# Optimization experiments

Hardware: AMD Instinct MI355X
Metric: run time of the kernel (lower is better)

## Reference

```python
import jax, jax.numpy as jnp
import numpy as np

CUTOFF = 3.0   # self.cutoff
RMIN = 3.5     # rmin in cutoff_function (note rmin > cutoff, faithful to source)
ETA = 4.0
N_RADIAL = 5
N_3BODY = 12
NATOMS = 2048
K = 48         # neighbors per atom (equal counts -> ragged loop becomes dense batch)
HID = 64
NPAIRS = NATOMS * K


def setup_inputs() -> dict:
    key = jax.random.key(0)
    ks = jax.random.split(key, 4)
    # displacements scaled so |rij| is mostly within a few Angstrom
    rij = jax.random.normal(ks[0], (NPAIRS, 3), jnp.float32) * 1.5
    # sorted-by-atom pair list with K neighbors per atom
    unique_i = jnp.repeat(jnp.arange(NATOMS, dtype=jnp.int64), K)
    W1 = jax.random.normal(ks[1], (N_RADIAL + N_3BODY, HID), jnp.float32) * 0.1
    b1 = jnp.zeros((HID,), jnp.float32)
    W2 = jax.random.normal(ks[2], (HID, HID), jnp.float32) * 0.1
    b2 = jnp.zeros((HID,), jnp.float32)
    W3 = jax.random.normal(ks[3], (HID, 1), jnp.float32) * 0.1
    b3 = jnp.zeros((1,), jnp.float32)
    return dict(rij=rij, unique_i=unique_i, W1=W1, b1=b1, W2=W2, b2=b2, W3=W3, b3=b3)


def _energy(rij, W1, b1, W2, b2, W3, b3):
    d = jnp.linalg.norm(rij, axis=1, keepdims=True)           # (P,1)
    diff_norm = rij / jnp.maximum(d, 1e-12)                   # F.normalize
    # pair cutoff (rmin=3.5, c=3.0 as in source)
    fc = jnp.where(d > RMIN,
                   0.5 + 0.5 * jnp.cos(jnp.pi * (d - RMIN) / (CUTOFF - RMIN)),
                   1.0)
    # radial Bessel basis, n = 1..5
    ns = jnp.arange(1, N_RADIAL + 1, dtype=rij.dtype)
    rbf = jnp.sqrt(2.0 / CUTOFF) * jnp.sin(ns * jnp.pi / CUTOFF * d) / d * fc  # (P,5)
    # 3-body Gaussian descriptors
    fcrik = (0.5 + 0.5 * jnp.cos(jnp.pi * d / CUTOFF))[:, 0]  # (P,)
    dn = diff_norm.reshape(NATOMS, K, 3)
    cosang = jnp.einsum('nkd,nld->nkl', dn, dn)               # (N,K,K) pairwise mm
    cosang = jnp.where(jnp.eye(K, dtype=bool)[None], 0.0, cosang)  # fill_diagonal_(0)
    mu = jnp.linspace(-1.0, 1.0, N_3BODY).astype(rij.dtype)
    w = fcrik.reshape(NATOMS, 1, K, 1)                        # fcrik broadcast on axis being summed
    g3b = jnp.sum(jnp.exp(-ETA * (cosang[..., None] - mu) ** 2) * w, axis=2)  # (N,K,12)
    g3b = g3b.reshape(NPAIRS, N_3BODY)
    desc = jnp.concatenate([rbf, g3b], axis=1)                # (P,17)
    h = jnp.tanh(desc @ W1 + b1)
    h = jnp.tanh(h @ W2 + b2)
    eij = h @ W3 + b3                                         # (P,1)
    return jnp.sum(eij * fc)


def reference(rij, unique_i, W1, b1, W2, b2, W3, b3):
    # Module output: gradients of total energy w.r.t. rij (written into beta)
    return jax.grad(_energy)(rij, W1, b1, W2, b2, W3, b3)
```

## Files before the change

### kernel.cpp

```cpp
#include <hip/hip_runtime.h>
#include <hip/hip_bf16.h>

#define NATOMS 2048
#define K 48
#define P (NATOMS * K)
#define NR 5
#define NM 12
#define ND 17
#define HID 64

#define PI_F 3.14159265358979f
#define CUT 3.0f
#define RMIN_F 3.5f
#define AFC (-6.28318530717959f)
#define POC (PI_F / CUT)
#define SQ 0.816496580927726f
#define E1C 1.45454545454545f
#define CMC (-0.132231404958678f)
#define N4L (-5.77078016355585f)
#define E1L (2.09846551402031f)
#define TL2 (2.88539008177793f)

__device__ unsigned short g_w1t[64 * 32];
__device__ unsigned short g_w2t[64 * 64];
__device__ unsigned short g_w2r[64 * 64];
__device__ unsigned short g_w1r[32 * 64];

using frag_ab = __attribute__((ext_vector_type(8))) short;
using frag_cd = __attribute__((ext_vector_type(4))) float;
using f2 = __attribute__((ext_vector_type(2))) float;
using f4 = __attribute__((ext_vector_type(4))) float;

__device__ __forceinline__ float fast_tanh(float x) {
    const float t = __builtin_amdgcn_exp2f(TL2 * x);
    return 1.0f - 2.0f * __builtin_amdgcn_rcpf(t + 1.0f);
}

__device__ __forceinline__ unsigned short f2bs(float x) {
    __hip_bfloat16 b = __float2bfloat16(x);
    return __builtin_bit_cast(unsigned short, b);
}

__device__ __forceinline__ float bs2f(unsigned short u) {
    return __builtin_bit_cast(float, ((unsigned)u) << 16);
}

template <int CTRL>
__device__ __forceinline__ float dpp_add(float x) {
    const int y = __builtin_amdgcn_update_dpp(
        0, __builtin_bit_cast(int, x), CTRL, 0xF, 0xF, true);
    return x + __builtin_bit_cast(float, y);
}

__global__ __launch_bounds__(256) void k_prep(const float* __restrict__ W1,
                                              const float* __restrict__ W2) {
    const int i = blockIdx.x * 256 + threadIdx.x;
    if (i < 2048) {
        const int n = i >> 5, k = i & 31;
        g_w1t[i] = (k < ND) ? f2bs(W1[k * HID + n]) : (unsigned short)0;
    } else if (i < 2048 + 4096) {
        const int j = i - 2048, n = j >> 6, k = j & 63;
        g_w2t[j] = f2bs(W2[k * HID + n]);
    } else if (i < 2048 + 8192) {
        const int j = i - (2048 + 4096);
        g_w2r[j] = f2bs(W2[j]);
    } else if (i < 2048 + 8192 + 2048) {
        const int j = i - (2048 + 8192), n = j >> 6;
        g_w1r[j] = (n < ND) ? f2bs(W1[j]) : (unsigned short)0;
    }
}

#define H1_OFF   0
#define ST_OFF   0
#define DESC_OFF 6912
#define GZ2_OFF  6912
#define SGD_OFF  6912
#define SGF_OFF  10560
#define SGU_OFF  11328
#define SS_OFF   13824
#define SE_OFF   18528
#define SU_OFF   19296
#define SFC_OFF  20064
#define SFK_OFF  20256
#define SM_BYTES 20448

__global__ __launch_bounds__(256, 6) void k_fused(const float* __restrict__ rij,
                                                  const float* __restrict__ b1,
                                                  const float* __restrict__ b2,
                                                  const float* __restrict__ W3,
                                                  const float* __restrict__ b3,
                                                  float* __restrict__ out) {
    __shared__ __align__(16) char smem[SM_BYTES];
    short*          h1S   = (short*)(smem + H1_OFF);
    unsigned short* sT    = (unsigned short*)(smem + ST_OFF);
    short*          descS = (short*)(smem + DESC_OFF);
    short*          gz2S  = (short*)(smem + GZ2_OFF);
    float*          sgd   = (float*)(smem + SGD_OFF);
    float*          sgf4  = (float*)(smem + SGF_OFF);
    float*          sgu4  = (float*)(smem + SGU_OFF);
    unsigned short* sS    = (unsigned short*)(smem + SS_OFF);
    float*          se    = (float*)(smem + SE_OFF);
    float*          su    = (float*)(smem + SU_OFF);
    float*          sfc   = (float*)(smem + SFC_OFF);
    float*          sfk   = (float*)(smem + SFK_OFF);

    const int t = threadIdx.x;
    const int base3 = blockIdx.x * (K * 3);
    const int w = t >> 6, lane = t & 63, quad = lane >> 4, lm = lane & 15;
    const int n0 = w * 16 + lm;

    const frag_ab wf1  = *(const frag_ab*)&g_w1t[n0 * 32 + quad * 8];
    const frag_ab wf2a = *(const frag_ab*)&g_w2t[n0 * 64 + quad * 8];
    const frag_ab wf2b = *(const frag_ab*)&g_w2t[n0 * 64 + 32 + quad * 8];
    const frag_ab wr2a = *(const frag_ab*)&g_w2r[n0 * 64 + quad * 8];
    const frag_ab wr2b = *(const frag_ab*)&g_w2r[n0 * 64 + 32 + quad * 8];
    const float bias1 = b1[n0];
    const float bias2 = b2[n0];
    const float w3n   = W3[n0];
    const float b3v   = b3[0];

    if (t < K) {
        const float x = rij[base3 + 3 * t];
        const float y = rij[base3 + 3 * t + 1];
        const float z = rij[base3 + 3 * t + 2];
        float s2 = fmaxf(x * x + y * y + z * z, 1e-24f);
        const float inv = __builtin_amdgcn_rsqf(s2);
        const float d = s2 * inv;
        *(f4*)&su[4 * t] = (f4){x * inv, y * inv, z * inv, d};
        sfk[t] = 0.5f + 0.5f * __cosf(POC * d);
        sfc[t] = (d > RMIN_F) ? (0.5f + 0.5f * __cosf(AFC * (d - RMIN_F))) : 1.0f;
#pragma unroll
        for (int c = ND; c < 32; c++) descS[t * 40 + c] = 0;
    }
    __syncthreads();

    if (t < 192) {
        const int k = t >> 2, ch = t & 3;
        const f4 uk = *(const f4*)&su[4 * k];
        const float* sul = &su[4 * (ch * 12)];
        f4 fkq[3];
        fkq[0] = *(const f4*)&sfk[ch * 12];
        fkq[1] = *(const f4*)&sfk[ch * 12 + 4];
        fkq[2] = *(const f4*)&sfk[ch * 12 + 8];
        f2 partv[6];
#pragma unroll
        for (int i = 0; i < 6; i++) partv[i] = (f2){0.0f, 0.0f};
#pragma unroll
        for (int li = 0; li < 12; li++) {
            const int l = ch * 12 + li;
            const f4 ul = *(const f4*)&sul[4 * li];
            float c = uk.x * ul.x + uk.y * ul.y + uk.z * ul.z;
            if (k == l) c = 0.0f;
            const float cp1 = c + 1.0f;
            const float e0 = __builtin_amdgcn_exp2f(N4L * cp1 * cp1) * fkq[li >> 2][li & 3];
            const float e1 = __builtin_amdgcn_exp2f(E1L * cp1);
            const float e2s = e1 * e1;
            const f2 e2v = {e2s, e2s};
            f2 tm = {e0, e0 * e1};
            partv[0] += tm;
#pragma unroll
            for (int i = 1; i < 6; i++) { tm *= e2v; partv[i] += tm; }
        }
#pragma unroll
        for (int i = 0; i < 6; i++) {
            partv[i].x = dpp_add<0x4E>(dpp_add<0xB1>(partv[i].x));
            partv[i].y = dpp_add<0x4E>(dpp_add<0xB1>(partv[i].y));
        }
        if (ch == 0) {
#pragma unroll
            for (int i = 0; i < 6; i++) {
                const int m0 = 2 * i, m1 = 2 * i + 1;
                descS[k * 40 + NR + m0] =
                    (short)f2bs(partv[i].x * __expf(CMC * (float)(m0 * m0)));
                descS[k * 40 + NR + m1] =
                    (short)f2bs(partv[i].y * __expf(CMC * (float)(m1 * m1)));
            }
        }
    } else {
#pragma unroll
        for (int r = 0; r < 4; r++) {
            const int idx = (t - 192) + 64 * r;
            if (idx < K * NR) {
                const int p = idx / NR, n = idx - NR * p;
                const float d = su[4 * p + 3];
                const float s = SQ * sfc[p] * __builtin_amdgcn_rcpf(d);
                descS[p * 40 + n] = (short)f2bs(s * __sinf((float)(n + 1) * POC * d));
            }
        }
    }
    __syncthreads();

    float t1[3][4];
    {
#pragma unroll
        for (int mt = 0; mt < 3; mt++) {
            const frag_ab a = *(const frag_ab*)&descS[(mt * 16 + lm) * 40 + quad * 8];
            frag_cd acc = {bias1, bias1, bias1, bias1};
            acc = __builtin_amdgcn_mfma_f32_16x16x32_bf16(a, wf1, acc, 0, 0, 0);
#pragma unroll
            for (int r = 0; r < 4; r++) {
                const float tv = fast_tanh(acc[r]);
                t1[mt][r] = tv;
                h1S[(mt * 16 + quad * 4 + r) * 72 + n0] = (short)f2bs(tv);
            }
        }
    }
    __syncthreads();

    {
#pragma unroll
        for (int mt = 0; mt < 3; mt++) {
            const frag_ab a0 = *(const frag_ab*)&h1S[(mt * 16 + lm) * 72 + quad * 8];
            const frag_ab a1 = *(const frag_ab*)&h1S[(mt * 16 + lm) * 72 + 32 + quad * 8];
            frag_cd acc = {bias2, bias2, bias2, bias2};
            acc = __builtin_amdgcn_mfma_f32_16x16x32_bf16(a0, wf2a, acc, 0, 0, 0);
            acc = __builtin_amdgcn_mfma_f32_16x16x32_bf16(a1, wf2b, acc, 0, 0, 0);
            const f4 fcv = *(const f4*)&sfc[mt * 16 + quad * 4];
            float ep[4];
#pragma unroll
            for (int r = 0; r < 4; r++) {
                const int row = mt * 16 + quad * 4 + r;
                const float tv = fast_tanh(acc[r]);
                ep[r] = tv * w3n;
                gz2S[row * 72 + n0] = (short)f2bs(fcv[r] * w3n * (1.0f - tv * tv));
            }
#pragma unroll
            for (int r = 0; r < 4; r++)
                ep[r] = dpp_add<0x118>(dpp_add<0x114>(dpp_add<0x112>(dpp_add<0x111>(ep[r]))));
            if (lm == 15) {
#pragma unroll
                for (int r = 0; r < 4; r++) se[w * 48 + mt * 16 + quad * 4 + r] = ep[r];
            }
        }
    }
    __syncthreads();

    {
#pragma unroll
        for (int mt = 0; mt < 3; mt++) {
            const frag_ab a0 = *(const frag_ab*)&gz2S[(mt * 16 + lm) * 72 + quad * 8];
            const frag_ab a1 = *(const frag_ab*)&gz2S[(mt * 16 + lm) * 72 + 32 + quad * 8];
            frag_cd acc = {0.0f, 0.0f, 0.0f, 0.0f};
            acc = __builtin_amdgcn_mfma_f32_16x16x32_bf16(a0, wr2a, acc, 0, 0, 0);
            acc = __builtin_amdgcn_mfma_f32_16x16x32_bf16(a1, wr2b, acc, 0, 0, 0);
#pragma unroll
            for (int r = 0; r < 4; r++) {
                const float g = acc[r] * (1.0f - t1[mt][r] * t1[mt][r]);
                h1S[(mt * 16 + quad * 4 + r) * 72 + n0] = (short)f2bs(g);
            }
        }
    }
    __syncthreads();

    for (int tid = w; tid < 6; tid += 4) {
        const int mt = tid >> 1, nt = tid & 1, n = nt * 16 + lm;
        const frag_ab b0 = *(const frag_ab*)&g_w1r[n * 64 + quad * 8];
        const frag_ab b1f = *(const frag_ab*)&g_w1r[n * 64 + 32 + quad * 8];
        const frag_ab a0 = *(const frag_ab*)&h1S[(mt * 16 + lm) * 72 + quad * 8];
        const frag_ab a1 = *(const frag_ab*)&h1S[(mt * 16 + lm) * 72 + 32 + quad * 8];
        frag_cd acc = {0.0f, 0.0f, 0.0f, 0.0f};
        acc = __builtin_amdgcn_mfma_f32_16x16x32_bf16(a0, b0, acc, 0, 0, 0);
        acc = __builtin_amdgcn_mfma_f32_16x16x32_bf16(a1, b1f, acc, 0, 0, 0);
        if (n < ND) {
            const int mm = n - NR;
            const float cmul = (n >= NR) ? __expf(CMC * (float)(mm * mm)) : 1.0f;
#pragma unroll
            for (int r = 0; r < 4; r++)
                sgd[(mt * 16 + quad * 4 + r) * 19 + n] = acc[r] * cmul;
        }
    }
    if (t < K)
        sgd[t * 19 + 17] = se[t] + se[48 + t] + se[96 + t] + se[144 + t] + b3v;
    __syncthreads();

    if (t < 192) {
        const int k = t >> 2, ch = t & 3;
        f2 gm[NM];
#pragma unroll
        for (int m = 0; m < NM; m++) {
            const float g = sgd[k * 19 + NR + m];
            gm[m] = (f2){g, (float)m * g};
        }
        const f4 uk = *(const f4*)&su[4 * k];
        const float* sul = &su[4 * (ch * 12)];
#pragma unroll
        for (int li = 0; li < 12; li++) {
            const int l = ch * 12 + li;
            const f4 ul = *(const f4*)&sul[4 * li];
            float c = uk.x * ul.x + uk.y * ul.y + uk.z * ul.z;
            if (k == l) c = 0.0f;
            const float cp1 = c + 1.0f;
            const float e0 = __builtin_amdgcn_exp2f(N4L * cp1 * cp1);
            const float x = __builtin_amdgcn_exp2f(E1L * cp1);
            const f2 xx = {x, x};
            f2 pd = gm[11];
#pragma unroll
            for (int m = 10; m >= 1; m--) pd = __builtin_elementwise_fma(pd, xx, gm[m]);
            const float Pv = fmaf(pd.x, x, gm[0].x);
            const float T = e0 * Pv;
            const float U = e0 * x * pd.y;
            const float Sp = fmaf(cp1, T, -(2.0f / 11.0f) * U);
            const float Sv = (k == l) ? 0.0f : (-8.0f) * Sp;
            sT[k * 49 + l] = f2bs(T);
            sS[k * 49 + l] = f2bs(Sv);
        }
    }
    __syncthreads();

    if (lane < K) {
        float s = 0.0f;
#pragma unroll
        for (int kk = 12 * w; kk < 12 * w + 12; kk++) s += bs2f(sT[kk * 49 + lane]);
        sgf4[w * 48 + lane] = s;

        const int k = lane;
        const float fk = sfk[k];
        float gx = 0.0f, gy = 0.0f, gz = 0.0f;
#pragma unroll
        for (int l = 12 * w; l < 12 * w + 12; l++) {
            const float wgt = fmaf(bs2f(sS[k * 49 + l]), sfk[l],
                                   bs2f(sS[l * 49 + k]) * fk);
            const f4 ul = *(const f4*)&su[4 * l];
            gx = fmaf(wgt, ul.x, gx);
            gy = fmaf(wgt, ul.y, gy);
            gz = fmaf(wgt, ul.z, gz);
        }
        sgu4[(w * 48 + k) * 3 + 0] = gx;
        sgu4[(w * 48 + k) * 3 + 1] = gy;
        sgu4[(w * 48 + k) * 3 + 2] = gz;
    }
    __syncthreads();

    if (t < K) {
        const float sgf_t = sgf4[t] + sgf4[48 + t] + sgf4[96 + t] + sgf4[144 + t];
        float gux = 0.0f, guy = 0.0f, guz = 0.0f;
#pragma unroll
        for (int ww = 0; ww < 4; ww++) {
            gux += sgu4[(ww * 48 + t) * 3 + 0];
            guy += sgu4[(ww * 48 + t) * 3 + 1];
            guz += sgu4[(ww * 48 + t) * 3 + 2];
        }
        const f4 uv = *(const f4*)&su[4 * t];
        const float d = uv.w;
        const float ux = uv.x, uy = uv.y, uz = uv.z;
        const float invd = __builtin_amdgcn_rcpf(d);
        float gfc = sgd[t * 19 + 17];
        float gdR = 0.0f;
#pragma unroll
        for (int n = 0; n < NR; n++) {
            const float bn = (float)(n + 1) * POC;
            float sn, cn;
            __sincosf(bn * d, &sn, &cn);
            const float g = sgd[t * 19 + n];
            gfc = fmaf(g, SQ * sn * invd, gfc);
            gdR = fmaf(g, SQ * (bn * cn - sn * invd) * invd, gdR);
        }
        const float fc = sfc[t];
        float dfc = 0.0f;
        if (d > RMIN_F) dfc = -0.5f * AFC * __sinf(AFC * (d - RMIN_F));
        const float dfcrik = -0.5f * POC * __sinf(POC * d);

        const float gd = fc * gdR + gfc * dfc + sgf_t * dfcrik;
        const float dot = gux * ux + guy * uy + guz * uz;

        out[base3 + 3 * t + 0] = fmaf(gd, ux, (gux - dot * ux) * invd);
        out[base3 + 3 * t + 1] = fmaf(gd, uy, (guy - dot * uy) * invd);
        out[base3 + 3 * t + 2] = fmaf(gd, uz, (guz - dot * uz) * invd);
    }
}

extern "C" void kernel_launch(void* const* d_in, const int* in_sizes, int n_in,
                              void* d_out, int out_size, void* d_ws, size_t ws_size,
                              hipStream_t stream) {
    (void)in_sizes; (void)n_in; (void)out_size; (void)d_ws; (void)ws_size;
    const float* rij = (const float*)d_in[0];
    const float* W1 = (const float*)d_in[2];
    const float* b1 = (const float*)d_in[3];
    const float* W2 = (const float*)d_in[4];
    const float* b2 = (const float*)d_in[5];
    const float* W3 = (const float*)d_in[6];
    const float* b3 = (const float*)d_in[7];
    float* out = (float*)d_out;

    k_prep<<<48, 256, 0, stream>>>(W1, W2);
    k_fused<<<NATOMS, 256, 0, stream>>>(rij, b1, b2, W3, b3, out);
}
```

Before: 93.52 us.

## Use 3 warps with row-owned MLP tiles, drop inter-layer barriers

Blocks shrink from 256 to 192 threads. Each wavefront now owns a 16-row slab of the 48 pairs and computes all 64 hidden columns itself, so the forward and backward MLP layers pass data only within a wave and several __syncthreads disappear. The eij reduction across hidden units now happens in registers through DPP instead of a cross-wave shared buffer. The radial sines are computed with a Chebyshev recurrence in the setup threads rather than by a separate thread group. In exchange, weight fragments are reloaded from global memory per tile, shared memory use grows, and the launch bound allows fewer blocks per CU.

```diff
diff --git a/kernel.cpp b/kernel.cpp
--- a/kernel.cpp
+++ b/kernel.cpp
@@ -3,7 +3,6 @@
 
 #define NATOMS 2048
 #define K 48
-#define P (NATOMS * K)
 #define NR 5
 #define NM 12
 #define ND 17
@@ -15,7 +14,6 @@
 #define AFC (-6.28318530717959f)
 #define POC (PI_F / CUT)
 #define SQ 0.816496580927726f
-#define E1C 1.45454545454545f
 #define CMC (-0.132231404958678f)
 #define N4L (-5.77078016355585f)
 #define E1L (2.09846551402031f)
@@ -71,20 +69,19 @@
 }
 
 #define H1_OFF   0
-#define ST_OFF   0
-#define DESC_OFF 6912
 #define GZ2_OFF  6912
-#define SGD_OFF  6912
-#define SGF_OFF  10560
-#define SGU_OFF  11328
-#define SS_OFF   13824
-#define SE_OFF   18528
-#define SU_OFF   19296
-#define SFC_OFF  20064
-#define SFK_OFF  20256
-#define SM_BYTES 20448
-
-__global__ __launch_bounds__(256, 6) void k_fused(const float* __restrict__ rij,
+#define SGF_OFF  6912
+#define SGU_OFF  7488
+#define DESC_OFF 13824
+#define SGD_OFF  13824
+#define SS_OFF   17664
+#define ST_OFF   22368
+#define SU_OFF   27072
+#define SFC_OFF  27840
+#define SFK_OFF  28032
+#define SM_BYTES 28224
+
+__global__ __launch_bounds__(192, 4) void k_fused(const float* __restrict__ rij,
                                                   const float* __restrict__ b1,
                                                   const float* __restrict__ b2,
                                                   const float* __restrict__ W3,
@@ -92,32 +89,30 @@
                                                   float* __restrict__ out) {
     __shared__ __align__(16) char smem[SM_BYTES];
     short*          h1S   = (short*)(smem + H1_OFF);
-    unsigned short* sT    = (unsigned short*)(smem + ST_OFF);
-    short*          descS = (short*)(smem + DESC_OFF);
     short*          gz2S  = (short*)(smem + GZ2_OFF);
-    float*          sgd   = (float*)(smem + SGD_OFF);
     float*          sgf4  = (float*)(smem + SGF_OFF);
     float*          sgu4  = (float*)(smem + SGU_OFF);
+    short*          descS = (short*)(smem + DESC_OFF);
+    float*          sgd   = (float*)(smem + SGD_OFF);
     unsigned short* sS    = (unsigned short*)(smem + SS_OFF);
-    float*          se    = (float*)(smem + SE_OFF);
+    unsigned short* sT    = (unsigned short*)(smem + ST_OFF);
     float*          su    = (float*)(smem + SU_OFF);
     float*          sfc   = (float*)(smem + SFC_OFF);
     float*          sfk   = (float*)(smem + SFK_OFF);
 
     const int t = threadIdx.x;
     const int base3 = blockIdx.x * (K * 3);
-    const int w = t >> 6, lane = t & 63, quad = lane >> 4, lm = lane & 15;
-    const int n0 = w * 16 + lm;
-
-    const frag_ab wf1  = *(const frag_ab*)&g_w1t[n0 * 32 + quad * 8];
-    const frag_ab wf2a = *(const frag_ab*)&g_w2t[n0 * 64 + quad * 8];
-    const frag_ab wf2b = *(const frag_ab*)&g_w2t[n0 * 64 + 32 + quad * 8];
-    const frag_ab wr2a = *(const frag_ab*)&g_w2r[n0 * 64 + quad * 8];
-    const frag_ab wr2b = *(const frag_ab*)&g_w2r[n0 * 64 + 32 + quad * 8];
-    const float bias1 = b1[n0];
-    const float bias2 = b2[n0];
-    const float w3n   = W3[n0];
-    const float b3v   = b3[0];
+    const int w0 = t >> 6, lane = t & 63, quad = lane >> 4, lm = lane & 15;
+    const int row0 = 16 * w0;
+
+    float b1v[4], b2v[4], w3v[4];
+#pragma unroll
+    for (int nt = 0; nt < 4; nt++) {
+        b1v[nt] = b1[nt * 16 + lm];
+        b2v[nt] = b2[nt * 16 + lm];
+        w3v[nt] = W3[nt * 16 + lm];
+    }
+    const float b3v = b3[0];
 
     if (t < K) {
         const float x = rij[base3 + 3 * t];
@@ -128,13 +123,25 @@
         const float d = s2 * inv;
         *(f4*)&su[4 * t] = (f4){x * inv, y * inv, z * inv, d};
         sfk[t] = 0.5f + 0.5f * __cosf(POC * d);
-        sfc[t] = (d > RMIN_F) ? (0.5f + 0.5f * __cosf(AFC * (d - RMIN_F))) : 1.0f;
+        const float fc = (d > RMIN_F) ? (0.5f + 0.5f * __cosf(AFC * (d - RMIN_F))) : 1.0f;
+        sfc[t] = fc;
+        float sn_, cn_;
+        __sincosf(POC * d, &sn_, &cn_);
+        const float sc = SQ * fc * inv;
+        const float c2 = 2.0f * cn_;
+        float sp = 0.0f, scur = sn_;
+#pragma unroll
+        for (int n = 0; n < NR; n++) {
+            descS[t * 40 + n] = (short)f2bs(sc * scur);
+            const float snx = c2 * scur - sp;
+            sp = scur; scur = snx;
+        }
 #pragma unroll
         for (int c = ND; c < 32; c++) descS[t * 40 + c] = 0;
     }
     __syncthreads();
 
-    if (t < 192) {
+    {
         const int k = t >> 2, ch = t & 3;
         const f4 uk = *(const f4*)&su[4 * k];
         const float* sul = &su[4 * (ch * 12)];
@@ -176,109 +183,102 @@
                     (short)f2bs(partv[i].y * __expf(CMC * (float)(m1 * m1)));
             }
         }
-    } else {
-#pragma unroll
-        for (int r = 0; r < 4; r++) {
-            const int idx = (t - 192) + 64 * r;
-            if (idx < K * NR) {
-                const int p = idx / NR, n = idx - NR * p;
-                const float d = su[4 * p + 3];
-                const float s = SQ * sfc[p] * __builtin_amdgcn_rcpf(d);
-                descS[p * 40 + n] = (short)f2bs(s * __sinf((float)(n + 1) * POC * d));
-            }
-        }
-    }
-    __syncthreads();
-
-    float t1[3][4];
-    {
-#pragma unroll
-        for (int mt = 0; mt < 3; mt++) {
-            const frag_ab a = *(const frag_ab*)&descS[(mt * 16 + lm) * 40 + quad * 8];
-            frag_cd acc = {bias1, bias1, bias1, bias1};
-            acc = __builtin_amdgcn_mfma_f32_16x16x32_bf16(a, wf1, acc, 0, 0, 0);
+    }
+
+    float t1v[4][4];
+    float eijr[4];
+
+    {
+        const frag_ab a = *(const frag_ab*)&descS[(row0 + lm) * 40 + quad * 8];
+#pragma unroll
+        for (int nt = 0; nt < 4; nt++) {
+            const frag_ab bfr = *(const frag_ab*)&g_w1t[(nt * 16 + lm) * 32 + quad * 8];
+            frag_cd acc = {b1v[nt], b1v[nt], b1v[nt], b1v[nt]};
+            acc = __builtin_amdgcn_mfma_f32_16x16x32_bf16(a, bfr, acc, 0, 0, 0);
 #pragma unroll
             for (int r = 0; r < 4; r++) {
                 const float tv = fast_tanh(acc[r]);
-                t1[mt][r] = tv;
-                h1S[(mt * 16 + quad * 4 + r) * 72 + n0] = (short)f2bs(tv);
-            }
-        }
-    }
-    __syncthreads();
-
-    {
-#pragma unroll
-        for (int mt = 0; mt < 3; mt++) {
-            const frag_ab a0 = *(const frag_ab*)&h1S[(mt * 16 + lm) * 72 + quad * 8];
-            const frag_ab a1 = *(const frag_ab*)&h1S[(mt * 16 + lm) * 72 + 32 + quad * 8];
-            frag_cd acc = {bias2, bias2, bias2, bias2};
-            acc = __builtin_amdgcn_mfma_f32_16x16x32_bf16(a0, wf2a, acc, 0, 0, 0);
-            acc = __builtin_amdgcn_mfma_f32_16x16x32_bf16(a1, wf2b, acc, 0, 0, 0);
-            const f4 fcv = *(const f4*)&sfc[mt * 16 + quad * 4];
-            float ep[4];
+                t1v[nt][r] = tv;
+                h1S[(row0 + quad * 4 + r) * 72 + nt * 16 + lm] = (short)f2bs(tv);
+            }
+        }
+    }
+
+    {
+        const frag_ab a0 = *(const frag_ab*)&h1S[(row0 + lm) * 72 + quad * 8];
+        const frag_ab a1 = *(const frag_ab*)&h1S[(row0 + lm) * 72 + 32 + quad * 8];
+        const f4 fcv = *(const f4*)&sfc[row0 + quad * 4];
+        float ep[4] = {0.0f, 0.0f, 0.0f, 0.0f};
+#pragma unroll
+        for (int nt = 0; nt < 4; nt++) {
+            const frag_ab b0 = *(const frag_ab*)&g_w2t[(nt * 16 + lm) * 64 + quad * 8];
+            const frag_ab b1f = *(const frag_ab*)&g_w2t[(nt * 16 + lm) * 64 + 32 + quad * 8];
+            frag_cd acc = {b2v[nt], b2v[nt], b2v[nt], b2v[nt]};
+            acc = __builtin_amdgcn_mfma_f32_16x16x32_bf16(a0, b0, acc, 0, 0, 0);
+            acc = __builtin_amdgcn_mfma_f32_16x16x32_bf16(a1, b1f, acc, 0, 0, 0);
 #pragma unroll
             for (int r = 0; r < 4; r++) {
-                const int row = mt * 16 + quad * 4 + r;
                 const float tv = fast_tanh(acc[r]);
-                ep[r] = tv * w3n;
-                gz2S[row * 72 + n0] = (short)f2bs(fcv[r] * w3n * (1.0f - tv * tv));
-            }
+                ep[r] = fmaf(tv, w3v[nt], ep[r]);
+                gz2S[(row0 + quad * 4 + r) * 72 + nt * 16 + lm] =
+                    (short)f2bs(fcv[r] * w3v[nt] * (1.0f - tv * tv));
+            }
+        }
+#pragma unroll
+        for (int r = 0; r < 4; r++)
+            eijr[r] = dpp_add<0x118>(dpp_add<0x114>(dpp_add<0x112>(dpp_add<0x111>(ep[r]))));
+    }
+
+    {
+        const frag_ab a0 = *(const frag_ab*)&gz2S[(row0 + lm) * 72 + quad * 8];
+        const frag_ab a1 = *(const frag_ab*)&gz2S[(row0 + lm) * 72 + 32 + quad * 8];
+#pragma unroll
+        for (int nt = 0; nt < 4; nt++) {
+            const frag_ab b0 = *(const frag_ab*)&g_w2r[(nt * 16 + lm) * 64 + quad * 8];
+            const frag_ab b1f = *(const frag_ab*)&g_w2r[(nt * 16 + lm) * 64 + 32 + quad * 8];
+            frag_cd acc = {0.0f, 0.0f, 0.0f, 0.0f};
+            acc = __builtin_amdgcn_mfma_f32_16x16x32_bf16(a0, b0, acc, 0, 0, 0);
+            acc = __builtin_amdgcn_mfma_f32_16x16x32_bf16(a1, b1f, acc, 0, 0, 0);
+#pragma unroll
+            for (int r = 0; r < 4; r++) {
+                const float g = acc[r] * (1.0f - t1v[nt][r] * t1v[nt][r]);
+                h1S[(row0 + quad * 4 + r) * 72 + nt * 16 + lm] = (short)f2bs(g);
+            }
+        }
+    }
+
+    {
+        const frag_ab a0 = *(const frag_ab*)&h1S[(row0 + lm) * 72 + quad * 8];
+        const frag_ab a1 = *(const frag_ab*)&h1S[(row0 + lm) * 72 + 32 + quad * 8];
+#pragma unroll
+        for (int nt = 0; nt < 2; nt++) {
+            const frag_ab b0 = *(const frag_ab*)&g_w1r[(nt * 16 + lm) * 64 + quad * 8];
+            const frag_ab b1f = *(const frag_ab*)&g_w1r[(nt * 16 + lm) * 64 + 32 + quad * 8];
+            frag_cd acc = {0.0f, 0.0f, 0.0f, 0.0f};
+            acc = __builtin_amdgcn_mfma_f32_16x16x32_bf16(a0, b0, acc, 0, 0, 0);
+            acc = __builtin_amdgcn_mfma_f32_16x16x32_bf16(a1, b1f, acc, 0, 0, 0);
+            const int n = nt * 16 + lm;
+            if (n < ND) {
+                const int mm = n - NR;
+                const float cmul = (n >= NR) ? __expf(CMC * (float)(mm * mm)) : 1.0f;
+#pragma unroll
+                for (int r = 0; r < 4; r++)
+                    sgd[(row0 + quad * 4 + r) * 20 + n] = acc[r] * cmul;
+            }
+        }
+        if (lm == 15) {
 #pragma unroll
             for (int r = 0; r < 4; r++)
-                ep[r] = dpp_add<0x118>(dpp_add<0x114>(dpp_add<0x112>(dpp_add<0x111>(ep[r]))));
-            if (lm == 15) {
-#pragma unroll
-                for (int r = 0; r < 4; r++) se[w * 48 + mt * 16 + quad * 4 + r] = ep[r];
-            }
-        }
-    }
-    __syncthreads();
-
-    {
-#pragma unroll
-        for (int mt = 0; mt < 3; mt++) {
-            const frag_ab a0 = *(const frag_ab*)&gz2S[(mt * 16 + lm) * 72 + quad * 8];
-            const frag_ab a1 = *(const frag_ab*)&gz2S[(mt * 16 + lm) * 72 + 32 + quad * 8];
-            frag_cd acc = {0.0f, 0.0f, 0.0f, 0.0f};
-            acc = __builtin_amdgcn_mfma_f32_16x16x32_bf16(a0, wr2a, acc, 0, 0, 0);
-            acc = __builtin_amdgcn_mfma_f32_16x16x32_bf16(a1, wr2b, acc, 0, 0, 0);
-#pragma unroll
-            for (int r = 0; r < 4; r++) {
-                const float g = acc[r] * (1.0f - t1[mt][r] * t1[mt][r]);
-                h1S[(mt * 16 + quad * 4 + r) * 72 + n0] = (short)f2bs(g);
-            }
-        }
-    }
-    __syncthreads();
-
-    for (int tid = w; tid < 6; tid += 4) {
-        const int mt = tid >> 1, nt = tid & 1, n = nt * 16 + lm;
-        const frag_ab b0 = *(const frag_ab*)&g_w1r[n * 64 + quad * 8];
-        const frag_ab b1f = *(const frag_ab*)&g_w1r[n * 64 + 32 + quad * 8];
-        const frag_ab a0 = *(const frag_ab*)&h1S[(mt * 16 + lm) * 72 + quad * 8];
-        const frag_ab a1 = *(const frag_ab*)&h1S[(mt * 16 + lm) * 72 + 32 + quad * 8];
-        frag_cd acc = {0.0f, 0.0f, 0.0f, 0.0f};
-        acc = __builtin_amdgcn_mfma_f32_16x16x32_bf16(a0, b0, acc, 0, 0, 0);
-        acc = __builtin_amdgcn_mfma_f32_16x16x32_bf16(a1, b1f, acc, 0, 0, 0);
-        if (n < ND) {
-            const int mm = n - NR;
-            const float cmul = (n >= NR) ? __expf(CMC * (float)(mm * mm)) : 1.0f;
-#pragma unroll
-            for (int r = 0; r < 4; r++)
-                sgd[(mt * 16 + quad * 4 + r) * 19 + n] = acc[r] * cmul;
-        }
-    }
-    if (t < K)
-        sgd[t * 19 + 17] = se[t] + se[48 + t] + se[96 + t] + se[144 + t] + b3v;
-    __syncthreads();
-
-    if (t < 192) {
+                sgd[(row0 + quad * 4 + r) * 20 + 17] = eijr[r] + b3v;
+        }
+    }
+
+    {
         const int k = t >> 2, ch = t & 3;
         f2 gm[NM];
 #pragma unroll
         for (int m = 0; m < NM; m++) {
-            const float g = sgd[k * 19 + NR + m];
+            const float g = sgd[k * 20 + NR + m];
             gm[m] = (f2){g, (float)m * g};
         }
         const f4 uk = *(const f4*)&su[4 * k];
@@ -310,14 +310,14 @@
     if (lane < K) {
         float s = 0.0f;
 #pragma unroll
-        for (int kk = 12 * w; kk < 12 * w + 12; kk++) s += bs2f(sT[kk * 49 + lane]);
-        sgf4[w * 48 + lane] = s;
+        for (int kk = 16 * w0; kk < 16 * w0 + 16; kk++) s += bs2f(sT[kk * 49 + lane]);
+        sgf4[w0 * 48 + lane] = s;
 
         const int k = lane;
         const float fk = sfk[k];
         float gx = 0.0f, gy = 0.0f, gz = 0.0f;
 #pragma unroll
-        for (int l = 12 * w; l < 12 * w + 12; l++) {
+        for (int l = 16 * w0; l < 16 * w0 + 16; l++) {
             const float wgt = fmaf(bs2f(sS[k * 49 + l]), sfk[l],
                                    bs2f(sS[l * 49 + k]) * fk);
             const f4 ul = *(const f4*)&su[4 * l];
@@ -325,17 +325,17 @@
             gy = fmaf(wgt, ul.y, gy);
             gz = fmaf(wgt, ul.z, gz);
         }
-        sgu4[(w * 48 + k) * 3 + 0] = gx;
-        sgu4[(w * 48 + k) * 3 + 1] = gy;
-        sgu4[(w * 48 + k) * 3 + 2] = gz;
+        sgu4[(w0 * 48 + k) * 3 + 0] = gx;
+        sgu4[(w0 * 48 + k) * 3 + 1] = gy;
+        sgu4[(w0 * 48 + k) * 3 + 2] = gz;
     }
     __syncthreads();
 
     if (t < K) {
-        const float sgf_t = sgf4[t] + sgf4[48 + t] + sgf4[96 + t] + sgf4[144 + t];
+        const float sgf_t = sgf4[t] + sgf4[48 + t] + sgf4[96 + t];
         float gux = 0.0f, guy = 0.0f, guz = 0.0f;
 #pragma unroll
-        for (int ww = 0; ww < 4; ww++) {
+        for (int ww = 0; ww < 3; ww++) {
             gux += sgu4[(ww * 48 + t) * 3 + 0];
             guy += sgu4[(ww * 48 + t) * 3 + 1];
             guz += sgu4[(ww * 48 + t) * 3 + 2];
@@ -344,14 +344,14 @@
         const float d = uv.w;
         const float ux = uv.x, uy = uv.y, uz = uv.z;
         const float invd = __builtin_amdgcn_rcpf(d);
-        float gfc = sgd[t * 19 + 17];
+        float gfc = sgd[t * 20 + 17];
         float gdR = 0.0f;
 #pragma unroll
         for (int n = 0; n < NR; n++) {
             const float bn = (float)(n + 1) * POC;
             float sn, cn;
             __sincosf(bn * d, &sn, &cn);
-            const float g = sgd[t * 19 + n];
+            const float g = sgd[t * 20 + n];
             gfc = fmaf(g, SQ * sn * invd, gfc);
             gdR = fmaf(g, SQ * (bn * cn - sn * invd) * invd, gdR);
         }
@@ -383,5 +383,5 @@
     float* out = (float*)d_out;
 
     k_prep<<<48, 256, 0, stream>>>(W1, W2);
-    k_fused<<<NATOMS, 256, 0, stream>>>(rij, b1, b2, W3, b3, out);
-}
+    k_fused<<<NATOMS, 192, 0, stream>>>(rij, b1, b2, W3, b3, out);
+}
```

Measured after the change: 94.78 us. Within noise of the previous version (+1.3%).
